# Kernel optimization log

Measured on AMD Instinct MI355X. Metric: run time of the kernel, lower is better.

Reference implementation:

```python
import jax, jax.numpy as jnp
import numpy as np

B, H, W = 64, 84, 84
IN_F, HID, NCLS = 128, 256, 50
C2 = IN_F * 2  # 256
EPS = 1e-5
K_NEIGH = 4


def _ring_edges(batch):
    rows = np.repeat(np.arange(batch), K_NEIGH)
    offs = np.tile(np.arange(1, K_NEIGH + 1), batch)
    cols = (rows + offs) % batch
    return jnp.asarray(np.stack([rows, cols]), dtype=jnp.int32)


def setup_inputs() -> dict:
    key = jax.random.key(0)
    ks = jax.random.split(key, 40)
    i = iter(range(40))
    def n(shape, s=0.05):
        return jax.random.normal(ks[next(i)], shape, jnp.float32) * s
    def u(shape):
        return jax.random.uniform(ks[next(i)], shape, jnp.float32, 0.5, 1.5)
    d = {}
    d['x'] = jax.random.normal(ks[next(i)], (B, 3, H, W), jnp.float32)
    # conv1 + bn1
    d['conv1_w'] = n((IN_F, 3, 3, 3)); d['conv1_b'] = n((IN_F,))
    d['bn1_g'] = 1.0 + n((IN_F,)); d['bn1_b'] = n((IN_F,))
    d['bn1_m'] = n((IN_F,)); d['bn1_v'] = u((IN_F,))
    # conv2 + bn2
    d['conv2_w'] = n((C2, IN_F, 3, 3)); d['conv2_b'] = n((C2,))
    d['bn2_g'] = 1.0 + n((C2,)); d['bn2_b'] = n((C2,))
    d['bn2_m'] = n((C2,)); d['bn2_v'] = u((C2,))
    # conv3 + bn3
    d['conv3_w'] = n((C2, C2, 3, 3)); d['conv3_b'] = n((C2,))
    d['bn3_g'] = 1.0 + n((C2,)); d['bn3_b'] = n((C2,))
    d['bn3_m'] = n((C2,)); d['bn3_v'] = u((C2,))
    # gcn1: Linear(256,256), attn Linear(512,1)
    d['gcn1_lw'] = n((HID, C2)); d['gcn1_lb'] = n((HID,))
    d['gcn1_aw'] = n((1, 2 * C2)); d['gcn1_ab'] = n((1,))
    # gcn2: Linear(256,256), attn Linear(512,1)
    d['gcn2_lw'] = n((HID, HID)); d['gcn2_lb'] = n((HID,))
    d['gcn2_aw'] = n((1, 2 * HID)); d['gcn2_ab'] = n((1,))
    # fc
    d['fc_w'] = n((NCLS, HID)); d['fc_b'] = n((NCLS,))
    d['edge_index'] = _ring_edges(B)  # [2, 4*B] deterministic ring graph
    return d


def _conv_bn_relu(x, w, b, g, be, m, v):
    y = jax.lax.conv_general_dilated(
        x, w, window_strides=(1, 1), padding='SAME',
        dimension_numbers=('NCHW', 'OIHW', 'NCHW')) + b[None, :, None, None]
    scale = (g / jnp.sqrt(v + EPS))[None, :, None, None]
    y = (y - m[None, :, None, None]) * scale + be[None, :, None, None]
    return jax.nn.relu(y)


def _gcn_conv(h, row, col, lw, lb, aw, ab):
    # h: [N, F]; edge gather -> attn MLP -> global softmax -> scatter-add
    ef = jnp.concatenate([h[row], h[col]], axis=1)          # [E, 2F]
    ew = jax.nn.leaky_relu(ef @ aw.T + ab, 0.01)            # [E, 1]
    ew = jax.nn.softmax(ew, axis=0)                          # softmax over all edges
    agg = jnp.zeros_like(h).at[row].add(h[col] * ew)        # [N, F]
    return agg @ lw.T + lb + h                               # linear + residual


def reference(x, conv1_w, conv1_b, bn1_g, bn1_b, bn1_m, bn1_v,
              conv2_w, conv2_b, bn2_g, bn2_b, bn2_m, bn2_v,
              conv3_w, conv3_b, bn3_g, bn3_b, bn3_m, bn3_v,
              gcn1_lw, gcn1_lb, gcn1_aw, gcn1_ab,
              gcn2_lw, gcn2_lb, gcn2_aw, gcn2_ab,
              fc_w, fc_b, edge_index):
    h = _conv_bn_relu(x, conv1_w, conv1_b, bn1_g, bn1_b, bn1_m, bn1_v)
    h = _conv_bn_relu(h, conv2_w, conv2_b, bn2_g, bn2_b, bn2_m, bn2_v)
    h = _conv_bn_relu(h, conv3_w, conv3_b, bn3_g, bn3_b, bn3_m, bn3_v)
    h = h.mean(axis=(2, 3))                                  # adaptive avg pool 1x1 + flatten -> [B, 256]
    row, col = edge_index[0], edge_index[1]
    h = jax.nn.relu(_gcn_conv(h, row, col, gcn1_lw, gcn1_lb, gcn1_aw, gcn1_ab))
    h = jax.nn.relu(_gcn_conv(h, row, col, gcn2_lw, gcn2_lb, gcn2_aw, gcn2_ab))
    return h @ fc_w.T + fc_b                                 # [B, 50]
```

## Files before the change

kernel.cpp:

```cpp
#include <hip/hip_runtime.h>
#include <hip/hip_bf16.h>

typedef __attribute__((ext_vector_type(8))) short bf16x8;
typedef __attribute__((ext_vector_type(4))) float f32x4;

#define DEV __device__ __forceinline__

static constexpr int Bn   = 64;
static constexpr int Hs   = 84;
static constexpr int HP   = 86;
static constexpr int C1c  = 128;
static constexpr int C2c  = 256;
static constexpr int NPOS = Hs * Hs;
static constexpr float EPSf = 1e-5f;

DEV __hip_bfloat16 f2b(float v) { return __float2bfloat16(v); }

DEV void gload16(const void* g, void* l) {
    __builtin_amdgcn_global_load_lds(
        (const __attribute__((address_space(1))) void*)g,
        (__attribute__((address_space(3))) void*)l, 16, 0, 0);
}

__global__ __launch_bounds__(128) void conv1_k(
    const float* __restrict__ x,
    const float* __restrict__ w,  const float* __restrict__ cb,
    const float* __restrict__ g,  const float* __restrict__ be,
    const float* __restrict__ mm, const float* __restrict__ vv,
    __hip_bfloat16* __restrict__ h1)
{
    __shared__ float xin[3][3][HP];
    int bi = blockIdx.x;
    int b = bi / Hs, y = bi % Hs;
    int t = threadIdx.x;

    for (int idx = t; idx < 3 * 3 * HP; idx += 128) {
        int ci = idx / (3 * HP);
        int r  = idx % (3 * HP);
        int dy = r / HP;
        int xx = r % HP;
        int iy = y + dy - 1;
        int ix = xx - 1;
        float v = 0.f;
        if (iy >= 0 && iy < Hs && ix >= 0 && ix < Hs)
            v = x[((size_t)(b * 3 + ci) * Hs + iy) * Hs + ix];
        xin[ci][dy][xx] = v;
    }
    int co = t;
    float wr[3][3][3];
    for (int ci = 0; ci < 3; ci++)
        for (int dy = 0; dy < 3; dy++)
            for (int dx = 0; dx < 3; dx++)
                wr[ci][dy][dx] = w[((co * 3 + ci) * 3 + dy) * 3 + dx];
    float scale = g[co] / sqrtf(vv[co] + EPSf);
    float bias  = (cb[co] - mm[co]) * scale + be[co];
    __syncthreads();

    for (int xp = 0; xp < Hs; xp++) {
        float acc = 0.f;
        #pragma unroll
        for (int ci = 0; ci < 3; ci++)
            #pragma unroll
            for (int dy = 0; dy < 3; dy++)
                #pragma unroll
                for (int dx = 0; dx < 3; dx++)
                    acc += xin[ci][dy][xp + dx] * wr[ci][dy][dx];
        float o = acc * scale + bias;
        o = o > 0.f ? o : 0.f;
        h1[((size_t)(b * HP + y + 1) * HP + (xp + 1)) * C1c + co] = f2b(o);
    }
}

template <int C>
__global__ void halo_zero(__hip_bfloat16* __restrict__ h)
{
    int i = blockIdx.x;
    int b = i / 340, p = i % 340;
    int y, xx;
    if (p < 86)       { y = 0;  xx = p; }
    else if (p < 172) { y = 85; xx = p - 86; }
    else if (p < 256) { xx = 0; y = p - 172 + 1; }
    else              { xx = 85; y = p - 256 + 1; }
    h[((size_t)(b * HP + y) * HP + xx) * C + threadIdx.x] = f2b(0.f);
}

template <int CIN>
__global__ void prep_w(const float* __restrict__ w, __hip_bfloat16* __restrict__ wm)
{
    int e  = blockIdx.x * 256 + threadIdx.x;
    int k  = e >> 8;
    int co = e & 255;
    int tap = k / CIN;
    int ci  = k % CIN;
    int ty = tap / 3, tx = tap % 3;
    wm[(size_t)(k >> 5) * 8192 + co * 32 + (k & 31)] =
        f2b(w[((size_t)(co * CIN + ci) * 3 + ty) * 3 + tx]);
}

__global__ void prep_sb(const float* __restrict__ cb, const float* __restrict__ g,
                        const float* __restrict__ be, const float* __restrict__ mm,
                        const float* __restrict__ vv, float* __restrict__ sb)
{
    int co = threadIdx.x;
    float s = g[co] / sqrtf(vv[co] + EPSf);
    sb[co] = s;
    sb[256 + co] = (cb[co] - mm[co]) * s + be[co];
}

__global__ void zero_f32(float* __restrict__ p)
{
    p[blockIdx.x * 256 + threadIdx.x] = 0.f;
}

template <int CIN, bool POOL>
__global__ __launch_bounds__(512, 2) void conv_igemm(
    const __hip_bfloat16* __restrict__ in, const __hip_bfloat16* __restrict__ wgt,
    const float* __restrict__ sb, __hip_bfloat16* __restrict__ out, float* __restrict__ pool)
{
    constexpr int KB = CIN / 32;
    constexpr int NK = 9 * KB / 2;
    constexpr unsigned BUFSZ = 65536u;
    __shared__ __align__(16) char lds[2 * 65536];
    __shared__ float pl[512];

    int t = threadIdx.x;
    int l = t & 63, w = t >> 6;
    int lidx = l & 15, lg = l >> 4;
    int wm = w >> 2, wn = w & 3;

    int nwg  = (int)gridDim.x;
    int orig = (int)blockIdx.x;
    int xcd = orig & 7, idx = orig >> 3;
    int q = nwg >> 3, r = nwg & 7;
    int bx = (xcd < r ? xcd * (q + 1) : r * (q + 1) + (xcd - r) * q) + idx;
    int m0 = bx * 256;

    int seg  = (t & 3) ^ ((t >> 3) & 3);
    int srow = t >> 2;
    const __hip_bfloat16 *pA0, *pA1;
    {
        int gm = m0 + srow;
        int b0 = gm / NPOS; int r0 = gm - b0 * NPOS;
        int y0 = r0 / Hs;   int x0 = r0 - y0 * Hs;
        pA0 = in + ((size_t)(b0 * HP + y0) * HP + x0) * CIN + seg * 8;
        gm = m0 + 128 + srow;
        b0 = gm / NPOS; r0 = gm - b0 * NPOS;
        y0 = r0 / Hs;   x0 = r0 - y0 * Hs;
        pA1 = in + ((size_t)(b0 * HP + y0) * HP + x0) * CIN + seg * 8;
    }
    const __hip_bfloat16* pB0 = wgt + (size_t)srow * 32 + seg * 8;
    const __hip_bfloat16* pB1 = wgt + (size_t)(128 + srow) * 32 + seg * 8;

    int swz = (lidx >> 1) & 3;
    unsigned aRd[8][2], bRd[4][2];
    #pragma unroll
    for (int mf = 0; mf < 8; mf++)
        #pragma unroll
        for (int kh = 0; kh < 2; kh++)
            aRd[mf][kh] = (unsigned)(kh * 16384 + (wm * 128 + mf * 16 + lidx) * 64 + ((lg ^ swz) * 16));
    #pragma unroll
    for (int nf = 0; nf < 4; nf++)
        #pragma unroll
        for (int kh = 0; kh < 2; kh++)
            bRd[nf][kh] = (unsigned)(32768 + kh * 16384 + (wn * 64 + nf * 16 + lidx) * 64 + ((lg ^ swz) * 16));

    f32x4 acc[8][4];
    #pragma unroll
    for (int i = 0; i < 8; i++)
        #pragma unroll
        for (int j = 0; j < 4; j++)
            acc[i][j] = (f32x4){0.f, 0.f, 0.f, 0.f};
    if (POOL) pl[t] = 0.f;

    auto AOFF = [&](int s) -> size_t {
        int kb = s / 9, tap = s - kb * 9;
        int ty = tap / 3, tx = tap - ty * 3;
        return (size_t)(ty * HP + tx) * CIN + kb * 32;
    };
    auto BOFF = [&](int s) -> size_t {
        int kb = s / 9, tap = s - kb * 9;
        return (size_t)(tap * KB + kb) * 8192;
    };
    auto ISSUE = [&](int kt2, int kh, unsigned bb) {
        int s = 2 * kt2 + kh;
        size_t ao = AOFF(s), bo = BOFF(s);
        unsigned ap = bb + (unsigned)(kh * 16384) + (unsigned)(w * 1024);
        unsigned bp = bb + 32768u + (unsigned)(kh * 16384) + (unsigned)(w * 1024);
        gload16(pA0 + ao, lds + ap);
        gload16(pA1 + ao, lds + ap + 8192);
        gload16(pB0 + bo, lds + bp);
        gload16(pB1 + bo, lds + bp + 8192);
    };

    ISSUE(0, 0, 0u);
    ISSUE(0, 1, 0u);

    for (int kt = 0; kt < NK; ++kt) {
        unsigned cb = (kt & 1) ? BUFSZ : 0u;
        unsigned nb = (kt & 1) ? 0u : BUFSZ;
        bool more = (kt + 1) < NK;

        asm volatile("s_waitcnt vmcnt(0)" ::: "memory");
        __builtin_amdgcn_s_barrier();
        asm volatile("" ::: "memory");

        {
            bf16x8 av[8], bv[4];
            #pragma unroll
            for (int mf = 0; mf < 8; mf++)
                av[mf] = *(const bf16x8*)(lds + cb + aRd[mf][0]);
            #pragma unroll
            for (int nf = 0; nf < 4; nf++)
                bv[nf] = *(const bf16x8*)(lds + cb + bRd[nf][0]);
            if (more) { ISSUE(kt + 1, 0, nb); ISSUE(kt + 1, 1, nb); }
            __builtin_amdgcn_s_setprio(1);
            #pragma unroll
            for (int mf = 0; mf < 8; mf++)
                #pragma unroll
                for (int nf = 0; nf < 4; nf++)
                    acc[mf][nf] = __builtin_amdgcn_mfma_f32_16x16x32_bf16(
                        av[mf], bv[nf], acc[mf][nf], 0, 0, 0);
            __builtin_amdgcn_s_setprio(0);
        }

        {
            bf16x8 av[8], bv[4];
            #pragma unroll
            for (int mf = 0; mf < 8; mf++)
                av[mf] = *(const bf16x8*)(lds + cb + aRd[mf][1]);
            #pragma unroll
            for (int nf = 0; nf < 4; nf++)
                bv[nf] = *(const bf16x8*)(lds + cb + bRd[nf][1]);
            __builtin_amdgcn_s_setprio(1);
            #pragma unroll
            for (int mf = 0; mf < 8; mf++)
                #pragma unroll
                for (int nf = 0; nf < 4; nf++)
                    acc[mf][nf] = __builtin_amdgcn_mfma_f32_16x16x32_bf16(
                        av[mf], bv[nf], acc[mf][nf], 0, 0, 0);
            __builtin_amdgcn_s_setprio(0);
        }
    }

    float sc[4], bi2[4];
    #pragma unroll
    for (int nf = 0; nf < 4; nf++) {
        int cn = wn * 64 + nf * 16 + lidx;
        sc[nf]  = sb[cn];
        bi2[nf] = sb[256 + cn];
    }

    if (!POOL) {
        #pragma unroll
        for (int mf = 0; mf < 8; mf++) {
            #pragma unroll
            for (int r2 = 0; r2 < 4; r2++) {
                int row = wm * 128 + mf * 16 + lg * 4 + r2;
                int gm2 = m0 + row;
                int b2  = gm2 / NPOS;
                int rm2 = gm2 - b2 * NPOS;
                int y2  = rm2 / Hs;
                int x2  = rm2 - y2 * Hs;
                size_t ob = ((size_t)(b2 * HP + y2 + 1) * HP + (x2 + 1)) * 256;
                #pragma unroll
                for (int nf = 0; nf < 4; nf++) {
                    float v = acc[mf][nf][r2] * sc[nf] + bi2[nf];
                    v = v > 0.f ? v : 0.f;
                    out[ob + wn * 64 + nf * 16 + lidx] = f2b(v);
                }
            }
        }
    } else {
        int bs_lo   = m0 / NPOS;
        int row_lim = (bs_lo + 1) * NPOS - m0;
        __builtin_amdgcn_s_barrier();
        #pragma unroll
        for (int nf = 0; nf < 4; nf++) {
            float s0 = 0.f, s1 = 0.f;
            #pragma unroll
            for (int mf = 0; mf < 8; mf++)
                #pragma unroll
                for (int r2 = 0; r2 < 4; r2++) {
                    int row = wm * 128 + mf * 16 + lg * 4 + r2;
                    float v = acc[mf][nf][r2] * sc[nf] + bi2[nf];
                    v = v > 0.f ? v : 0.f;
                    if (row < row_lim) s0 += v; else s1 += v;
                }
            int cl = wn * 64 + nf * 16 + lidx;
            atomicAdd(&pl[cl], s0);
            if (row_lim < 256) atomicAdd(&pl[256 + cl], s1);
        }
        __syncthreads();
        if (t < 256)
            atomicAdd(&pool[bs_lo * 256 + t], pl[t]);
        else if (row_lim < 256)
            atomicAdd(&pool[(bs_lo + 1) * 256 + (t - 256)], pl[t]);
    }
}

__global__ void pool_div(const float* __restrict__ pool, float* __restrict__ h0)
{
    int i = blockIdx.x * 256 + threadIdx.x;
    h0[i] = pool[i] * (1.0f / (float)NPOS);
}

__global__ __launch_bounds__(256) void gcn_attn(
    const float* __restrict__ h, const float* __restrict__ aw,
    const float* __restrict__ ab, const int* __restrict__ ei,
    float* __restrict__ ew)
{
    __shared__ float p[64], q[64], red[256];
    int t = threadIdx.x;
    if (t < 64) {
        float pp = 0.f, qq = 0.f;
        for (int c = 0; c < 256; c++) {
            float hv = h[t * 256 + c];
            pp += hv * aw[c];
            qq += hv * aw[256 + c];
        }
        p[t] = pp; q[t] = qq;
    }
    __syncthreads();
    int r = ei[t], c = ei[256 + t];
    float s = p[r] + q[c] + ab[0];
    s = s >= 0.f ? s : 0.01f * s;
    red[t] = s;
    __syncthreads();
    for (int st = 128; st > 0; st >>= 1) {
        if (t < st) red[t] = fmaxf(red[t], red[t + st]);
        __syncthreads();
    }
    float mx = red[0];
    __syncthreads();
    float e = expf(s - mx);
    red[t] = e;
    __syncthreads();
    for (int st = 128; st > 0; st >>= 1) {
        if (t < st) red[t] += red[t + st];
        __syncthreads();
    }
    ew[t] = e / red[0];
}

__global__ __launch_bounds__(256) void gcn_agg(
    const float* __restrict__ h, const float* __restrict__ ew, const int* __restrict__ ei,
    const float* __restrict__ lw, const float* __restrict__ lb,
    float* __restrict__ ho)
{
    __shared__ float agg[256];
    __shared__ float ewl[256];
    __shared__ int rl[256], cl[256];
    int n = blockIdx.x;
    int t = threadIdx.x;
    ewl[t] = ew[t];
    rl[t] = ei[t];
    cl[t] = ei[256 + t];
    __syncthreads();
    float a = 0.f;
    for (int e = 0; e < 256; e++)
        if (rl[e] == n) a += ewl[e] * h[cl[e] * 256 + t];
    agg[t] = a;
    __syncthreads();
    float o = 0.f;
    for (int c2 = 0; c2 < 256; c2++)
        o += agg[c2] * lw[t * 256 + c2];
    o += lb[t] + h[n * 256 + t];
    o = o > 0.f ? o : 0.f;
    ho[n * 256 + t] = o;
}

__global__ void fc_k(const float* __restrict__ h, const float* __restrict__ fw,
                     const float* __restrict__ fb, float* __restrict__ out)
{
    int n = blockIdx.x;
    int t = threadIdx.x;
    if (t < 50) {
        float o = 0.f;
        for (int c = 0; c < 256; c++)
            o += h[n * 256 + c] * fw[t * 256 + c];
        o += fb[t];
        out[n * 50 + t] = o;
    }
}

extern "C" void kernel_launch(void* const* d_in, const int* in_sizes, int n_in,
                              void* d_out, int out_size, void* d_ws, size_t ws_size,
                              hipStream_t stream)
{
    (void)in_sizes; (void)n_in; (void)out_size;

    const float* X    = (const float*)d_in[0];
    const float* c1w  = (const float*)d_in[1];
    const float* c1b  = (const float*)d_in[2];
    const float* b1g  = (const float*)d_in[3];
    const float* b1b  = (const float*)d_in[4];
    const float* b1m  = (const float*)d_in[5];
    const float* b1v  = (const float*)d_in[6];
    const float* c2w  = (const float*)d_in[7];
    const float* c2b  = (const float*)d_in[8];
    const float* b2g  = (const float*)d_in[9];
    const float* b2b  = (const float*)d_in[10];
    const float* b2m  = (const float*)d_in[11];
    const float* b2v  = (const float*)d_in[12];
    const float* c3w  = (const float*)d_in[13];
    const float* c3b  = (const float*)d_in[14];
    const float* b3g  = (const float*)d_in[15];
    const float* b3b  = (const float*)d_in[16];
    const float* b3m  = (const float*)d_in[17];
    const float* b3v  = (const float*)d_in[18];
    const float* g1lw = (const float*)d_in[19];
    const float* g1lb = (const float*)d_in[20];
    const float* g1aw = (const float*)d_in[21];
    const float* g1ab = (const float*)d_in[22];
    const float* g2lw = (const float*)d_in[23];
    const float* g2lb = (const float*)d_in[24];
    const float* g2aw = (const float*)d_in[25];
    const float* g2ab = (const float*)d_in[26];
    const float* fcw  = (const float*)d_in[27];
    const float* fcb  = (const float*)d_in[28];
    const int*   EI   = (const int*)d_in[29];

    size_t fixedB = 3000000;
    int chb = 16;
    if (ws_size >= (size_t)64 * 5680128 + fixedB)      chb = 64;
    else if (ws_size >= (size_t)32 * 5680128 + fixedB) chb = 32;
    int nchunks = Bn / chb;
    int mch = chb * NPOS;

    char* p = (char*)d_ws;
    auto carve = [&](size_t bytes) {
        char* r = p;
        p += (bytes + 255) & ~(size_t)255;
        return r;
    };
    __hip_bfloat16* h1c = (__hip_bfloat16*)carve((size_t)chb * HP * HP * C1c * 2);
    __hip_bfloat16* h2c = (__hip_bfloat16*)carve((size_t)chb * HP * HP * C2c * 2);
    __hip_bfloat16* wm2 = (__hip_bfloat16*)carve((size_t)9 * C1c * 256 * 2);
    __hip_bfloat16* wm3 = (__hip_bfloat16*)carve((size_t)9 * C2c * 256 * 2);
    float* sb2  = (float*)carve(512 * 4);
    float* sb3  = (float*)carve(512 * 4);
    float* pool = (float*)carve(64 * 256 * 4);
    float* h0   = (float*)carve(64 * 256 * 4);
    float* hg1  = (float*)carve(64 * 256 * 4);
    float* hg2  = (float*)carve(64 * 256 * 4);
    float* ew1  = (float*)carve(256 * 4);
    float* ew2  = (float*)carve(256 * 4);

    halo_zero<C1c><<<dim3(chb * 340), dim3(C1c), 0, stream>>>(h1c);
    halo_zero<C2c><<<dim3(chb * 340), dim3(C2c), 0, stream>>>(h2c);
    prep_w<C1c><<<dim3(9 * C1c), dim3(256), 0, stream>>>(c2w, wm2);
    prep_w<C2c><<<dim3(9 * C2c), dim3(256), 0, stream>>>(c3w, wm3);
    prep_sb<<<dim3(1), dim3(256), 0, stream>>>(c2b, b2g, b2b, b2m, b2v, sb2);
    prep_sb<<<dim3(1), dim3(256), 0, stream>>>(c3b, b3g, b3b, b3m, b3v, sb3);
    zero_f32<<<dim3(64), dim3(256), 0, stream>>>(pool);

    for (int ch = 0; ch < nchunks; ch++) {
        const float* xch = X + (size_t)ch * chb * 3 * NPOS;
        conv1_k<<<dim3(chb * Hs), dim3(C1c), 0, stream>>>(
            xch, c1w, c1b, b1g, b1b, b1m, b1v, h1c);
        conv_igemm<C1c, false><<<dim3(mch / 256), dim3(512), 0, stream>>>(
            h1c, wm2, sb2, h2c, nullptr);
        conv_igemm<C2c, true ><<<dim3(mch / 256), dim3(512), 0, stream>>>(
            h2c, wm3, sb3, nullptr, pool + (size_t)ch * chb * 256);
    }
    pool_div<<<dim3(64), dim3(256), 0, stream>>>(pool, h0);

    gcn_attn<<<dim3(1), dim3(256), 0, stream>>>(h0, g1aw, g1ab, EI, ew1);
    gcn_agg<<<dim3(64), dim3(256), 0, stream>>>(h0, ew1, EI, g1lw, g1lb, hg1);
    gcn_attn<<<dim3(1), dim3(256), 0, stream>>>(hg1, g2aw, g2ab, EI, ew2);
    gcn_agg<<<dim3(64), dim3(256), 0, stream>>>(hg1, ew2, EI, g2lw, g2lb, hg2);
    fc_k<<<dim3(64), dim3(64), 0, stream>>>(hg2, fcw, fcb, (float*)d_out);
}
```

Before: 909.1 us.

## Load conv weight fragments directly to registers, halve LDS double buffer

The implicit-GEMM conv kernel no longer stages the weight (B) tile through LDS. Each wave loads its B fragments straight from global memory into registers one k-step ahead, and LDS keeps only the A tiles, so the buffer is halved. This cuts LDS traffic and footprint, which could allow more resident workgroups. In exchange, direct global loads of weights are less coalesced, add register pressure, and their latency is now covered only by the vmcnt wait at the loop top.

New measurement: 1.013 ms. +11.4%, slower.

```diff
diff --git a/kernel.cpp b/kernel.cpp
--- a/kernel.cpp
+++ b/kernel.cpp
@@ -119,8 +119,8 @@
 {
     constexpr int KB = CIN / 32;
     constexpr int NK = 9 * KB / 2;
-    constexpr unsigned BUFSZ = 65536u;
-    __shared__ __align__(16) char lds[2 * 65536];
+    constexpr unsigned BUFSZ = 32768u;
+    __shared__ __align__(16) char lds[2 * 32768];
     __shared__ float pl[512];
 
     int t = threadIdx.x;
@@ -148,21 +148,16 @@
         y0 = r0 / Hs;   x0 = r0 - y0 * Hs;
         pA1 = in + ((size_t)(b0 * HP + y0) * HP + x0) * CIN + seg * 8;
     }
-    const __hip_bfloat16* pB0 = wgt + (size_t)srow * 32 + seg * 8;
-    const __hip_bfloat16* pB1 = wgt + (size_t)(128 + srow) * 32 + seg * 8;
+
+    const __hip_bfloat16* pBF = wgt + (size_t)((wn * 64 + lidx) * 32 + lg * 8);
 
     int swz = (lidx >> 1) & 3;
-    unsigned aRd[8][2], bRd[4][2];
+    unsigned aRd[8][2];
     #pragma unroll
     for (int mf = 0; mf < 8; mf++)
         #pragma unroll
         for (int kh = 0; kh < 2; kh++)
             aRd[mf][kh] = (unsigned)(kh * 16384 + (wm * 128 + mf * 16 + lidx) * 64 + ((lg ^ swz) * 16));
-    #pragma unroll
-    for (int nf = 0; nf < 4; nf++)
-        #pragma unroll
-        for (int kh = 0; kh < 2; kh++)
-            bRd[nf][kh] = (unsigned)(32768 + kh * 16384 + (wn * 64 + nf * 16 + lidx) * 64 + ((lg ^ swz) * 16));
 
     f32x4 acc[8][4];
     #pragma unroll
@@ -181,19 +176,23 @@
         int kb = s / 9, tap = s - kb * 9;
         return (size_t)(tap * KB + kb) * 8192;
     };
-    auto ISSUE = [&](int kt2, int kh, unsigned bb) {
+    auto ISSUE_A = [&](int kt2, int kh, unsigned bb) {
         int s = 2 * kt2 + kh;
-        size_t ao = AOFF(s), bo = BOFF(s);
+        size_t ao = AOFF(s);
         unsigned ap = bb + (unsigned)(kh * 16384) + (unsigned)(w * 1024);
-        unsigned bp = bb + 32768u + (unsigned)(kh * 16384) + (unsigned)(w * 1024);
         gload16(pA0 + ao, lds + ap);
         gload16(pA1 + ao, lds + ap + 8192);
-        gload16(pB0 + bo, lds + bp);
-        gload16(pB1 + bo, lds + bp + 8192);
     };
 
-    ISSUE(0, 0, 0u);
-    ISSUE(0, 1, 0u);
+    ISSUE_A(0, 0, 0u);
+    ISSUE_A(0, 1, 0u);
+    bf16x8 bvA[4], bvB[4];
+    {
+        size_t bo = BOFF(0);
+        #pragma unroll
+        for (int nf = 0; nf < 4; nf++)
+            bvA[nf] = *(const bf16x8*)(pBF + bo + nf * 512);
+    }
 
     for (int kt = 0; kt < NK; ++kt) {
         unsigned cb = (kt & 1) ? BUFSZ : 0u;
@@ -205,39 +204,46 @@
         asm volatile("" ::: "memory");
 
         {
-            bf16x8 av[8], bv[4];
+            bf16x8 av[8];
             #pragma unroll
             for (int mf = 0; mf < 8; mf++)
                 av[mf] = *(const bf16x8*)(lds + cb + aRd[mf][0]);
+            size_t bo1 = BOFF(2 * kt + 1);
             #pragma unroll
             for (int nf = 0; nf < 4; nf++)
-                bv[nf] = *(const bf16x8*)(lds + cb + bRd[nf][0]);
-            if (more) { ISSUE(kt + 1, 0, nb); ISSUE(kt + 1, 1, nb); }
+                bvB[nf] = *(const bf16x8*)(pBF + bo1 + nf * 512);
+            if (more) ISSUE_A(kt + 1, 0, nb);
+            __builtin_amdgcn_sched_barrier(0);
             __builtin_amdgcn_s_setprio(1);
             #pragma unroll
             for (int mf = 0; mf < 8; mf++)
                 #pragma unroll
                 for (int nf = 0; nf < 4; nf++)
                     acc[mf][nf] = __builtin_amdgcn_mfma_f32_16x16x32_bf16(
-                        av[mf], bv[nf], acc[mf][nf], 0, 0, 0);
+                        av[mf], bvA[nf], acc[mf][nf], 0, 0, 0);
             __builtin_amdgcn_s_setprio(0);
         }
 
         {
-            bf16x8 av[8], bv[4];
+            bf16x8 av[8];
             #pragma unroll
             for (int mf = 0; mf < 8; mf++)
                 av[mf] = *(const bf16x8*)(lds + cb + aRd[mf][1]);
-            #pragma unroll
-            for (int nf = 0; nf < 4; nf++)
-                bv[nf] = *(const bf16x8*)(lds + cb + bRd[nf][1]);
+            if (more) {
+                size_t bo2 = BOFF(2 * kt + 2);
+                #pragma unroll
+                for (int nf = 0; nf < 4; nf++)
+                    bvA[nf] = *(const bf16x8*)(pBF + bo2 + nf * 512);
+                ISSUE_A(kt + 1, 1, nb);
+            }
+            __builtin_amdgcn_sched_barrier(0);
             __builtin_amdgcn_s_setprio(1);
             #pragma unroll
             for (int mf = 0; mf < 8; mf++)
                 #pragma unroll
                 for (int nf = 0; nf < 4; nf++)
                     acc[mf][nf] = __builtin_amdgcn_mfma_f32_16x16x32_bf16(
-                        av[mf], bv[nf], acc[mf][nf], 0, 0, 0);
+                        av[mf], bvB[nf], acc[mf][nf], 0, 0, 0);
             __builtin_amdgcn_s_setprio(0);
         }
     }
```
